# Optimization experiments

Measured on AMD Instinct MI355X. Metric: run time of the kernel, lower is better.

The kernel has to match this reference:

```python
import jax, jax.numpy as jnp
import numpy as np

D_MODEL = 1024
NUM_HEADS = 16
HEAD_DIM = D_MODEL // NUM_HEADS
THETA = 10000.0
B, S = 2, 2048


def setup_inputs() -> dict:
    key = jax.random.key(0)
    ks = jax.random.split(key, 9)
    std = 1.0 / np.sqrt(D_MODEL)
    x = jax.random.normal(ks[0], (B, S, D_MODEL), dtype=jnp.float32)
    Wq = jax.random.normal(ks[1], (D_MODEL, D_MODEL), dtype=jnp.float32) * std
    Wk = jax.random.normal(ks[2], (D_MODEL, D_MODEL), dtype=jnp.float32) * std
    Wv = jax.random.normal(ks[3], (D_MODEL, D_MODEL), dtype=jnp.float32) * std
    Wo = jax.random.normal(ks[4], (D_MODEL, D_MODEL), dtype=jnp.float32) * std
    bq = jax.random.normal(ks[5], (D_MODEL,), dtype=jnp.float32) * std
    bk = jax.random.normal(ks[6], (D_MODEL,), dtype=jnp.float32) * std
    bv = jax.random.normal(ks[7], (D_MODEL,), dtype=jnp.float32) * std
    bo = jax.random.normal(ks[8], (D_MODEL,), dtype=jnp.float32) * std
    return {"x": x, "Wq": Wq, "bq": bq, "Wk": Wk, "bk": bk,
            "Wv": Wv, "bv": bv, "Wo": Wo, "bo": bo}


def _apply_rope(t, cos, sin):
    # t: [B, H, S, hd]; cos/sin: [S, hd//2]; interleaved-pair rotation
    t1 = t[..., 0::2]
    t2 = t[..., 1::2]
    r1 = t1 * cos - t2 * sin
    r2 = t1 * sin + t2 * cos
    return jnp.stack([r1, r2], axis=-1).reshape(t.shape)


def reference(x, Wq, bq, Wk, bk, Wv, bv, Wo, bo):
    B_, S_, D = x.shape
    H, hd = NUM_HEADS, HEAD_DIM
    # QKV projections (nn.Linear: x @ W.T + b)
    q = (x @ Wq.T + bq).reshape(B_, S_, H, hd).transpose(0, 2, 1, 3)  # [B,H,S,hd]
    k = (x @ Wk.T + bk).reshape(B_, S_, H, hd).transpose(0, 2, 1, 3)
    v = (x @ Wv.T + bv).reshape(B_, S_, H, hd).transpose(0, 2, 1, 3)
    # RoPE with token_positions = arange(S)
    pos = jnp.arange(S_, dtype=jnp.float32)
    inv_freq = 1.0 / (THETA ** (jnp.arange(0, hd, 2, dtype=jnp.float32) / hd))
    ang = pos[:, None] * inv_freq[None, :]  # [S, hd//2]
    cos, sin = jnp.cos(ang), jnp.sin(ang)
    q = _apply_rope(q, cos, sin)
    k = _apply_rope(k, cos, sin)
    # causal scaled-dot-product attention
    scores = jnp.einsum('bhqd,bhkd->bhqk', q, k) / jnp.sqrt(jnp.asarray(hd, x.dtype))
    causal = jnp.arange(S_)[:, None] >= jnp.arange(S_)[None, :]  # [S,S]
    scores = jnp.where(causal, scores, -jnp.inf)
    attn = jax.nn.softmax(scores, axis=-1)
    out = jnp.einsum('bhqk,bhkd->bhqd', attn, v)  # [B,H,S,hd]
    out = out.transpose(0, 2, 1, 3).reshape(B_, S_, D)
    return out @ Wo.T + bo
```

## Files before the change

kernel.cpp:

```cpp
#include <hip/hip_runtime.h>
#include <hip/hip_bf16.h>
#include <stdint.h>

typedef __bf16 bf16_t;
typedef __bf16 bf16x4 __attribute__((ext_vector_type(4)));
typedef __bf16 bf16x8 __attribute__((ext_vector_type(8)));
typedef float  f32x4  __attribute__((ext_vector_type(4)));

#define DM    1024
#define NH    16
#define HD    64
#define SEQ   2048
#define BATCH 2
#define BS    (BATCH*SEQ)
#define NQKV  (3*DM)

#define GLOAD_LDS16(g, l) \
  __builtin_amdgcn_global_load_lds((const __attribute__((address_space(1))) void*)(g), \
                                   (__attribute__((address_space(3))) void*)(l), 16, 0, 0)

__device__ __forceinline__ f32x4 mfma16(bf16x8 a, bf16x8 b, f32x4 c) {
  return __builtin_amdgcn_mfma_f32_16x16x32_bf16(a, b, c, 0, 0, 0);
}

__device__ __forceinline__ bf16x8 vcat(uint2 a, uint2 b) {
  union { uint32_t w[4]; bf16x8 v; } u;
  u.w[0] = a.x; u.w[1] = a.y; u.w[2] = b.x; u.w[3] = b.y;
  return u.v;
}

__global__ __launch_bounds__(256) void k_cast_all(
    const float* __restrict__ x,  const float* __restrict__ Wq,
    const float* __restrict__ Wk, const float* __restrict__ Wv,
    const float* __restrict__ Wo, const float* __restrict__ bq,
    const float* __restrict__ bk, const float* __restrict__ bv,
    bf16_t* __restrict__ xb, bf16_t* __restrict__ Wcat,
    bf16_t* __restrict__ Wob, float* __restrict__ bcat,
    float2* __restrict__ rt)
{
  const int bid = blockIdx.x, tid = threadIdx.x;
  if (bid >= 4099) {
    const int idx = (bid - 4099) * 256 + tid;
    const int s = idx >> 5, i = idx & 31;
    float inv = powf(10000.0f, -(float)(2 * i) / 64.0f);
    float ang = (float)s * inv;
    rt[idx] = make_float2(cosf(ang), sinf(ang));
    return;
  }
  if (bid >= 4096) {
    const int k = bid - 4096;
    const float* src = (k == 0) ? bq : (k == 1) ? bk : bv;
    *(float4*)&bcat[k * DM + tid * 4] = *(const float4*)&src[tid * 4];
    return;
  }
  const float* src; bf16_t* dst; int i;
  if (bid < 2048)      { src = x;  dst = xb;                i = bid * 2048 + tid * 8; }
  else if (bid < 2560) { src = Wq; dst = Wcat;              i = (bid - 2048) * 2048 + tid * 8; }
  else if (bid < 3072) { src = Wk; dst = Wcat + DM * DM;    i = (bid - 2560) * 2048 + tid * 8; }
  else if (bid < 3584) { src = Wv; dst = Wcat + 2 * DM * DM;i = (bid - 3072) * 2048 + tid * 8; }
  else                 { src = Wo; dst = Wob;               i = (bid - 3584) * 2048 + tid * 8; }
  float4 a = *(const float4*)(src + i);
  float4 b = *(const float4*)(src + i + 4);
  bf16x8 o;
  o[0] = (bf16_t)a.x; o[1] = (bf16_t)a.y; o[2] = (bf16_t)a.z; o[3] = (bf16_t)a.w;
  o[4] = (bf16_t)b.x; o[5] = (bf16_t)b.y; o[6] = (bf16_t)b.z; o[7] = (bf16_t)b.w;
  *(bf16x8*)(dst + i) = o;
}

__global__ __launch_bounds__(256) void k_gemm_qk(
    const bf16_t* __restrict__ A, const bf16_t* __restrict__ B,
    const float* __restrict__ bias, const float2* __restrict__ rt,
    bf16_t* __restrict__ Qo, bf16_t* __restrict__ Ko)
{
  const int K = DM;
  __shared__ __align__(16) bf16_t As[128 * 32];
  __shared__ __align__(16) bf16_t Bs[128 * 32];
  const int tid  = threadIdx.x;
  const int lane = tid & 63;
  const int wave = tid >> 6;
  const int wr = wave >> 1, wc = wave & 1;
  const int m0 = blockIdx.y * 128, n0 = blockIdx.x * 128;
  const int c16 = lane & 15, g = lane >> 4;

  f32x4 acc[4][4];
  #pragma unroll
  for (int i = 0; i < 4; ++i)
    #pragma unroll
    for (int j = 0; j < 4; ++j)
      #pragma unroll
      for (int e = 0; e < 4; ++e) acc[i][j][e] = 0.0f;

  const int srow = wave * 32;
  const int lrow = lane >> 2;
  const int lk   = (lane & 3) * 8;
  const bf16_t* ga0 = A + (size_t)(m0 + srow +      lrow) * K + lk;
  const bf16_t* ga1 = A + (size_t)(m0 + srow + 16 + lrow) * K + lk;
  const bf16_t* gb0 = B + (size_t)(n0 + srow +      lrow) * K + lk;
  const bf16_t* gb1 = B + (size_t)(n0 + srow + 16 + lrow) * K + lk;
  bf16_t* la0 = &As[(srow)      * 32];
  bf16_t* la1 = &As[(srow + 16) * 32];
  bf16_t* lb0 = &Bs[(srow)      * 32];
  bf16_t* lb1 = &Bs[(srow + 16) * 32];

  const bf16_t* pa = &As[(wr * 64 + c16) * 32 + g * 8];
  const bf16_t* pb = &Bs[(wc * 64 + c16) * 32 + g * 8];

  for (int kt = 0; kt < K; kt += 32) {
    GLOAD_LDS16(ga0 + kt, la0);
    GLOAD_LDS16(ga1 + kt, la1);
    GLOAD_LDS16(gb0 + kt, lb0);
    GLOAD_LDS16(gb1 + kt, lb1);
    __syncthreads();
    bf16x8 af[4], bfr[4];
    #pragma unroll
    for (int t = 0; t < 4; ++t) af[t]  = *(const bf16x8*)(pa + t * 16 * 32);
    #pragma unroll
    for (int t = 0; t < 4; ++t) bfr[t] = *(const bf16x8*)(pb + t * 16 * 32);
    #pragma unroll
    for (int i = 0; i < 4; ++i)
      #pragma unroll
      for (int j = 0; j < 4; ++j)
        acc[i][j] = mfma16(bfr[j], af[i], acc[i][j]);
    __syncthreads();
  }

  const int region = n0 >> 10;
  bf16_t* dst = region ? Ko : Qo;
  const float qs = region ? 1.0f : (0.125f * 1.44269504088896f);
  #pragma unroll
  for (int j = 0; j < 4; ++j) {
    const int nb = n0 + wc * 64 + j * 16 + (g << 2);
    const float4 bv = *(const float4*)&bias[nb];
    const int h  = (nb >> 6) & 15;
    const int d0 = nb & 63;
    #pragma unroll
    for (int i = 0; i < 4; ++i) {
      const int m = m0 + wr * 64 + i * 16 + c16;
      const int s = m & 2047;
      const int bh = ((m >> 11) << 4) + h;
      const float4 cs = *(const float4*)&rt[(size_t)s * 32 + (d0 >> 1)];
      const float v0 = acc[i][j][0] + bv.x;
      const float v1 = acc[i][j][1] + bv.y;
      const float v2 = acc[i][j][2] + bv.z;
      const float v3 = acc[i][j][3] + bv.w;
      bf16x4 ov;
      ov[0] = (bf16_t)((v0 * cs.x - v1 * cs.y) * qs);
      ov[1] = (bf16_t)((v0 * cs.y + v1 * cs.x) * qs);
      ov[2] = (bf16_t)((v2 * cs.z - v3 * cs.w) * qs);
      ov[3] = (bf16_t)((v2 * cs.w + v3 * cs.z) * qs);
      *(bf16x4*)&dst[((size_t)bh * SEQ + s) * HD + d0] = ov;
    }
  }
}

__global__ __launch_bounds__(256) void k_gemm_v(
    const bf16_t* __restrict__ A, const bf16_t* __restrict__ B,
    const float* __restrict__ bias, bf16_t* __restrict__ Vt)
{
  const int K = DM;
  __shared__ __align__(16) bf16_t As[128 * 32];
  __shared__ __align__(16) bf16_t Bs[128 * 32];
  const int tid  = threadIdx.x;
  const int lane = tid & 63;
  const int wave = tid >> 6;
  const int wr = wave >> 1, wc = wave & 1;
  const int m0 = blockIdx.y * 128, n0 = blockIdx.x * 128;
  const int c16 = lane & 15, g = lane >> 4;

  f32x4 acc[4][4];
  #pragma unroll
  for (int i = 0; i < 4; ++i)
    #pragma unroll
    for (int j = 0; j < 4; ++j)
      #pragma unroll
      for (int e = 0; e < 4; ++e) acc[i][j][e] = 0.0f;

  const int srow = wave * 32;
  const int lrow = lane >> 2;
  const int lk   = (lane & 3) * 8;
  const bf16_t* ga0 = A + (size_t)(m0 + srow +      lrow) * K + lk;
  const bf16_t* ga1 = A + (size_t)(m0 + srow + 16 + lrow) * K + lk;
  const bf16_t* gb0 = B + (size_t)(n0 + srow +      lrow) * K + lk;
  const bf16_t* gb1 = B + (size_t)(n0 + srow + 16 + lrow) * K + lk;
  bf16_t* la0 = &As[(srow)      * 32];
  bf16_t* la1 = &As[(srow + 16) * 32];
  bf16_t* lb0 = &Bs[(srow)      * 32];
  bf16_t* lb1 = &Bs[(srow + 16) * 32];

  const bf16_t* pa = &As[(wr * 64 + c16) * 32 + g * 8];
  const bf16_t* pb = &Bs[(wc * 64 + c16) * 32 + g * 8];

  for (int kt = 0; kt < K; kt += 32) {
    GLOAD_LDS16(ga0 + kt, la0);
    GLOAD_LDS16(ga1 + kt, la1);
    GLOAD_LDS16(gb0 + kt, lb0);
    GLOAD_LDS16(gb1 + kt, lb1);
    __syncthreads();
    bf16x8 af[4], bfr[4];
    #pragma unroll
    for (int t = 0; t < 4; ++t) af[t]  = *(const bf16x8*)(pa + t * 16 * 32);
    #pragma unroll
    for (int t = 0; t < 4; ++t) bfr[t] = *(const bf16x8*)(pb + t * 16 * 32);
    #pragma unroll
    for (int i = 0; i < 4; ++i)
      #pragma unroll
      for (int j = 0; j < 4; ++j)
        acc[i][j] = mfma16(af[i], bfr[j], acc[i][j]);
    __syncthreads();
  }

  const int rbase = m0 + wr * 64 + (g << 2);
  const int cbase = n0 + wc * 64 + c16;
  #pragma unroll
  for (int j = 0; j < 4; ++j) {
    const int c = cbase + j * 16;
    const float bv = bias[c];
    const int h = (c >> 6) & 15;
    const int d = c & 63;
    #pragma unroll
    for (int i = 0; i < 4; ++i) {
      bf16x4 ov;
      #pragma unroll
      for (int e = 0; e < 4; ++e) ov[e] = (bf16_t)(acc[i][j][e] + bv);
      const int r0 = rbase + i * 16;
      const int bh = ((r0 >> 11) << 4) + h;
      *(bf16x4*)&Vt[((size_t)bh * HD + d) * SEQ + (r0 & 2047)] = ov;
    }
  }
}

__global__ __launch_bounds__(512) void k_gemm_out(
    const bf16_t* __restrict__ A, const bf16_t* __restrict__ B,
    const float* __restrict__ bias, float* __restrict__ C)
{
  const int K = DM, N = DM;
  __shared__ __align__(16) bf16_t As[128 * 32];
  __shared__ __align__(16) bf16_t Bs[128 * 32];
  const int tid  = threadIdx.x;
  const int lane = tid & 63;
  const int w    = tid >> 6;
  const int wr = w >> 2, wc = w & 3;
  const int m0 = blockIdx.y * 128, n0 = blockIdx.x * 128;
  const int c16 = lane & 15, g = lane >> 4;

  f32x4 acc[4][2];
  #pragma unroll
  for (int i = 0; i < 4; ++i)
    #pragma unroll
    for (int j = 0; j < 2; ++j)
      #pragma unroll
      for (int e = 0; e < 4; ++e) acc[i][j][e] = 0.0f;

  const int lrow = lane >> 2;
  const int lk   = (lane & 3) * 8;
  const bf16_t* ga = A + (size_t)(m0 + w * 16 + lrow) * K + lk;
  const bf16_t* gb = B + (size_t)(n0 + w * 16 + lrow) * K + lk;
  bf16_t* la = &As[(w * 16) * 32];
  bf16_t* lb = &Bs[(w * 16) * 32];

  const bf16_t* pa = &As[(wr * 64 + c16) * 32 + g * 8];
  const bf16_t* pb = &Bs[(wc * 32 + c16) * 32 + g * 8];

  for (int kt = 0; kt < K; kt += 32) {
    GLOAD_LDS16(ga + kt, la);
    GLOAD_LDS16(gb + kt, lb);
    __syncthreads();
    bf16x8 af[4], bfr[2];
    #pragma unroll
    for (int t = 0; t < 4; ++t) af[t]  = *(const bf16x8*)(pa + t * 16 * 32);
    #pragma unroll
    for (int t = 0; t < 2; ++t) bfr[t] = *(const bf16x8*)(pb + t * 16 * 32);
    #pragma unroll
    for (int i = 0; i < 4; ++i)
      #pragma unroll
      for (int j = 0; j < 2; ++j)
        acc[i][j] = mfma16(af[i], bfr[j], acc[i][j]);
    __syncthreads();
  }

  const int rbase = m0 + wr * 64 + (g << 2);
  const int cbase = n0 + wc * 32 + c16;
  #pragma unroll
  for (int j = 0; j < 2; ++j) {
    const int c = cbase + j * 16;
    const float bv = bias[c];
    #pragma unroll
    for (int i = 0; i < 4; ++i) {
      #pragma unroll
      for (int e = 0; e < 4; ++e) {
        const int r = rbase + i * 16 + e;
        C[(size_t)r * N + c] = acc[i][j][e] + bv;
      }
    }
  }
}

__global__ __launch_bounds__(256, 4) void k_attn(
    const bf16_t* __restrict__ Q, const bf16_t* __restrict__ K,
    const bf16_t* __restrict__ Vt, bf16_t* __restrict__ O)
{
  __shared__ __align__(16) bf16_t kbuf[2][64 * 64];
  __shared__ __align__(16) bf16_t vbuf[2][64 * 64];
  const int tid = threadIdx.x, lane = tid & 63, w = tid >> 6;
  const int qt = 31 - (blockIdx.x >> 5);
  const int bh = blockIdx.x & 31;
  const int b  = bh >> 4, h = bh & 15;
  const int q0 = qt * 64 + w * 16;
  const int c16 = lane & 15;
  const int g   = lane >> 4;
  const int q   = q0 + c16;

  const bf16_t* Qb = Q  + (size_t)bh * SEQ * HD;
  const bf16_t* Kb = K  + (size_t)bh * SEQ * HD;
  const bf16_t* Vb = Vt + (size_t)bh * HD * SEQ;

  bf16x8 qf0 = *(const bf16x8*)&Qb[(size_t)q * HD + g * 8];
  bf16x8 qf1 = *(const bf16x8*)&Qb[(size_t)q * HD + 32 + g * 8];

  f32x4 oacc[4];
  #pragma unroll
  for (int dblk = 0; dblk < 4; ++dblk)
    #pragma unroll
    for (int e = 0; e < 4; ++e) oacc[dblk][e] = 0.0f;
  float m_ = -1e30f, l_ = 0.0f;

  const int ntile = qt + 1;

  const int soff0 = w * 1024 + lane * 16;
  const int soff1 = soff0 + 4096;
  const int srow0 = soff0 >> 7, srow1 = soff1 >> 7;
  const int scb0  = (soff0 & 127) ^ ((srow0 & 7) << 4);
  const int scb1  = (soff1 & 127) ^ ((srow1 & 7) << 4);
  const bf16_t* gk0 = &Kb[(size_t)srow0 * HD + (scb0 >> 1)];
  const bf16_t* gk1 = &Kb[(size_t)srow1 * HD + (scb1 >> 1)];
  const bf16_t* gv0 = &Vb[(size_t)srow0 * SEQ + (scb0 >> 1)];
  const bf16_t* gv1 = &Vb[(size_t)srow1 * SEQ + (scb1 >> 1)];
  bf16_t* lk0A = &kbuf[0][(w * 1024) >> 1];
  bf16_t* lk1A = &kbuf[0][(w * 1024 + 4096) >> 1];
  bf16_t* lk0B = &kbuf[1][(w * 1024) >> 1];
  bf16_t* lk1B = &kbuf[1][(w * 1024 + 4096) >> 1];
  bf16_t* lv0A = &vbuf[0][(w * 1024) >> 1];
  bf16_t* lv1A = &vbuf[0][(w * 1024 + 4096) >> 1];
  bf16_t* lv0B = &vbuf[1][(w * 1024) >> 1];
  bf16_t* lv1B = &vbuf[1][(w * 1024 + 4096) >> 1];

  const int sw = (c16 & 7) << 4;
  const int e0 = ((16 * g) ^ sw) >> 1;
  const int dhi = (((64 + 16 * g) ^ sw) >> 1) - e0;
  const bf16_t* kp0 = &kbuf[0][c16 * 64 + e0];
  const bf16_t* kp1 = &kbuf[1][c16 * 64 + e0];
  const int ve0 = ((8 * g) ^ sw) >> 1;
  const int ve1 = ((32 + 8 * g) ^ sw) >> 1;
  const int ve2 = ((64 + 8 * g) ^ sw) >> 1;
  const int ve3 = ((96 + 8 * g) ^ sw) >> 1;
  const bf16_t* vp0 = &vbuf[0][c16 * 64];
  const bf16_t* vp1 = &vbuf[1][c16 * 64];

  GLOAD_LDS16(gk0, lk0A); GLOAD_LDS16(gk1, lk1A);
  GLOAD_LDS16(gv0, lv0A); GLOAD_LDS16(gv1, lv1A);
  gk0 += 4096; gk1 += 4096; gv0 += 64; gv1 += 64;
  __syncthreads();

  for (int t = 0; t < ntile; ++t) {
    const bool odd = t & 1;
    if (t + 1 < ntile) {
      GLOAD_LDS16(gk0, odd ? lk0A : lk0B); GLOAD_LDS16(gk1, odd ? lk1A : lk1B);
      GLOAD_LDS16(gv0, odd ? lv0A : lv0B); GLOAD_LDS16(gv1, odd ? lv1A : lv1B);
      gk0 += 4096; gk1 += 4096; gv0 += 64; gv1 += 64;
    }

    const bf16_t* kp = odd ? kp1 : kp0;
    const bf16_t* vp = odd ? vp1 : vp0;

    f32x4 st[4];
    __builtin_amdgcn_s_setprio(1);
    #pragma unroll
    for (int u = 0; u < 4; ++u) {
      bf16x8 k0 = *(const bf16x8*)(kp + u * 1024);
      bf16x8 k1 = *(const bf16x8*)(kp + u * 1024 + dhi);
      f32x4 z; z[0] = z[1] = z[2] = z[3] = 0.0f;
      z = mfma16(k0, qf0, z);
      z = mfma16(k1, qf1, z);
      st[u] = z;
    }
    __builtin_amdgcn_s_setprio(0);

    bf16x8 vlo[4], vhi[4];
    #pragma unroll
    for (int dblk = 0; dblk < 4; ++dblk) {
      const bf16_t* vpb = vp + dblk * 1024;
      uint2 a0 = *(const uint2*)(vpb + ve0);
      uint2 a1 = *(const uint2*)(vpb + ve1);
      uint2 a2 = *(const uint2*)(vpb + ve2);
      uint2 a3 = *(const uint2*)(vpb + ve3);
      vlo[dblk] = vcat(a0, a1);
      vhi[dblk] = vcat(a2, a3);
    }

    float pv[16];
    if (t == qt) {
      const int kv0 = t * 64;
      #pragma unroll
      for (int u = 0; u < 4; ++u)
        #pragma unroll
        for (int r = 0; r < 4; ++r) {
          const int kv = kv0 + 16 * u + 4 * g + r;
          pv[u * 4 + r] = (kv <= q) ? st[u][r] : -1e30f;
        }
    } else {
      #pragma unroll
      for (int u = 0; u < 4; ++u)
        #pragma unroll
        for (int r = 0; r < 4; ++r)
          pv[u * 4 + r] = st[u][r];
    }

    float ma = fmaxf(fmaxf(pv[0], pv[1]), fmaxf(pv[2], pv[3]));
    float mb = fmaxf(fmaxf(pv[4], pv[5]), fmaxf(pv[6], pv[7]));
    float mc = fmaxf(fmaxf(pv[8], pv[9]), fmaxf(pv[10], pv[11]));
    float md = fmaxf(fmaxf(pv[12], pv[13]), fmaxf(pv[14], pv[15]));
    const float lmx = fmaxf(fmaxf(ma, mb), fmaxf(mc, md));

    if (__any(lmx - m_ > 12.0f)) {
      float mx = fmaxf(lmx, __shfl_xor(lmx, 16));
      mx = fmaxf(mx, __shfl_xor(mx, 32));
      const float mn = fmaxf(m_, mx);
      const float alpha = exp2f(m_ - mn);
      l_ *= alpha;
      #pragma unroll
      for (int dblk = 0; dblk < 4; ++dblk)
        #pragma unroll
        for (int e = 0; e < 4; ++e) oacc[dblk][e] *= alpha;
      m_ = mn;
    }

    #pragma unroll
    for (int i = 0; i < 16; ++i) pv[i] = exp2f(pv[i] - m_);
    float s0 = (pv[0] + pv[1]) + (pv[2] + pv[3]);
    float s1 = (pv[4] + pv[5]) + (pv[6] + pv[7]);
    float s2 = (pv[8] + pv[9]) + (pv[10] + pv[11]);
    float s3 = (pv[12] + pv[13]) + (pv[14] + pv[15]);
    l_ += (s0 + s1) + (s2 + s3);

    bf16x8 pf0, pf1;
    #pragma unroll
    for (int j = 0; j < 8; ++j) {
      pf0[j] = (bf16_t)pv[j];
      pf1[j] = (bf16_t)pv[8 + j];
    }

    __builtin_amdgcn_s_setprio(1);
    #pragma unroll
    for (int dblk = 0; dblk < 4; ++dblk) {
      oacc[dblk] = mfma16(vlo[dblk], pf0, oacc[dblk]);
      oacc[dblk] = mfma16(vhi[dblk], pf1, oacc[dblk]);
    }
    __builtin_amdgcn_s_setprio(0);

    __syncthreads();
  }

  l_ += __shfl_xor(l_, 16);
  l_ += __shfl_xor(l_, 32);
  const float inv = 1.0f / l_;
  bf16_t* orow = O + ((size_t)(b * SEQ + q)) * DM + h * HD;
  #pragma unroll
  for (int dblk = 0; dblk < 4; ++dblk) {
    bf16x4 ov;
    #pragma unroll
    for (int r = 0; r < 4; ++r) ov[r] = (bf16_t)(oacc[dblk][r] * inv);
    *(bf16x4*)&orow[dblk * 16 + 4 * g] = ov;
  }
}

extern "C" void kernel_launch(void* const* d_in, const int* in_sizes, int n_in,
                              void* d_out, int out_size, void* d_ws, size_t ws_size,
                              hipStream_t stream)
{
  const float* x  = (const float*)d_in[0];
  const float* Wq = (const float*)d_in[1];
  const float* bq = (const float*)d_in[2];
  const float* Wk = (const float*)d_in[3];
  const float* bk = (const float*)d_in[4];
  const float* Wv = (const float*)d_in[5];
  const float* bv = (const float*)d_in[6];
  const float* Wo = (const float*)d_in[7];
  const float* bo = (const float*)d_in[8];
  float* out = (float*)d_out;

  char* ws = (char*)d_ws;
  size_t off = 0;
  auto alloc = [&](size_t bytes) { char* p = ws + off; off += (bytes + 255) & ~255ULL; return p; };
  bf16_t* xb   = (bf16_t*)alloc((size_t)BS * DM * 2);
  bf16_t* Wcat = (bf16_t*)alloc((size_t)NQKV * DM * 2);
  bf16_t* Wob  = (bf16_t*)alloc((size_t)DM * DM * 2);
  float*  bcat = (float*)alloc((size_t)NQKV * 4);
  float2* rt   = (float2*)alloc((size_t)SEQ * 32 * 8);
  bf16_t* Qh   = (bf16_t*)alloc((size_t)BS * DM * 2);
  bf16_t* Kh   = (bf16_t*)alloc((size_t)BS * DM * 2);
  bf16_t* Vth  = (bf16_t*)alloc((size_t)BS * DM * 2);
  bf16_t* Oh   = (bf16_t*)alloc((size_t)BS * DM * 2);
  (void)ws_size; (void)in_sizes; (void)n_in; (void)out_size;

  k_cast_all<<<4099 + 256, 256, 0, stream>>>(x, Wq, Wk, Wv, Wo, bq, bk, bv,
                                             xb, Wcat, Wob, bcat, rt);

  dim3 gqk(16, 32);
  k_gemm_qk<<<gqk, 256, 0, stream>>>(xb, Wcat, bcat, rt, Qh, Kh);
  dim3 gv(8, 32);
  k_gemm_v<<<gv, 256, 0, stream>>>(xb, Wcat + 2 * DM * DM, bcat + 2 * DM, Vth);
  k_attn<<<32 * 32, 256, 0, stream>>>(Qh, Kh, Vth, Oh);
  dim3 g2(DM / 128, BS / 128);
  k_gemm_out<<<g2, 512, 0, stream>>>(Oh, Wob, bo, out);
}
```

Measured before the change: 129.5 us.

## Permute V-transpose sequence layout for 16-byte LDS reads; reorder attention tile schedule

The V projection epilogue now writes Vt with a permuted sequence order inside each 64-wide block, so that in the attention kernel each lane's eight needed V elements are contiguous. Each lane can then fetch them with one 16-byte LDS read in place of four 8-byte reads plus a register concatenation. The same swizzle offsets used for K are reused for V. Separately, the mapping from block index to query tile changes from strictly descending to a zig-zag over four rounds, which changes how causal work is spread across the launch order.

```diff
diff --git a/kernel.cpp b/kernel.cpp
--- a/kernel.cpp
+++ b/kernel.cpp
@@ -21,12 +21,6 @@
 
 __device__ __forceinline__ f32x4 mfma16(bf16x8 a, bf16x8 b, f32x4 c) {
   return __builtin_amdgcn_mfma_f32_16x16x32_bf16(a, b, c, 0, 0, 0);
-}
-
-__device__ __forceinline__ bf16x8 vcat(uint2 a, uint2 b) {
-  union { uint32_t w[4]; bf16x8 v; } u;
-  u.w[0] = a.x; u.w[1] = a.y; u.w[2] = b.x; u.w[3] = b.y;
-  return u.v;
 }
 
 __global__ __launch_bounds__(256) void k_cast_all(
@@ -224,7 +218,10 @@
       for (int e = 0; e < 4; ++e) ov[e] = (bf16_t)(acc[i][j][e] + bv);
       const int r0 = rbase + i * 16;
       const int bh = ((r0 >> 11) << 4) + h;
-      *(bf16x4*)&Vt[((size_t)bh * HD + d) * SEQ + (r0 & 2047)] = ov;
+      const int s0 = r0 & 2047;
+      const int u  = (s0 >> 4) & 3;
+      const int p0 = (s0 & ~63) + ((u >> 1) << 5) + (g << 3) + ((u & 1) << 2);
+      *(bf16x4*)&Vt[((size_t)bh * HD + d) * SEQ + p0] = ov;
     }
   }
 }
@@ -302,8 +299,10 @@
   __shared__ __align__(16) bf16_t kbuf[2][64 * 64];
   __shared__ __align__(16) bf16_t vbuf[2][64 * 64];
   const int tid = threadIdx.x, lane = tid & 63, w = tid >> 6;
-  const int qt = 31 - (blockIdx.x >> 5);
+  const int rr = blockIdx.x >> 8;
+  const int kk = (blockIdx.x >> 5) & 7;
   const int bh = blockIdx.x & 31;
+  const int qt = (rr == 0) ? kk : (rr == 1) ? 15 - kk : (rr == 2) ? 16 + kk : 31 - kk;
   const int b  = bh >> 4, h = bh & 15;
   const int q0 = qt * 64 + w * 16;
   const int c16 = lane & 15;
@@ -349,12 +348,8 @@
   const int dhi = (((64 + 16 * g) ^ sw) >> 1) - e0;
   const bf16_t* kp0 = &kbuf[0][c16 * 64 + e0];
   const bf16_t* kp1 = &kbuf[1][c16 * 64 + e0];
-  const int ve0 = ((8 * g) ^ sw) >> 1;
-  const int ve1 = ((32 + 8 * g) ^ sw) >> 1;
-  const int ve2 = ((64 + 8 * g) ^ sw) >> 1;
-  const int ve3 = ((96 + 8 * g) ^ sw) >> 1;
-  const bf16_t* vp0 = &vbuf[0][c16 * 64];
-  const bf16_t* vp1 = &vbuf[1][c16 * 64];
+  const bf16_t* vp0 = &vbuf[0][c16 * 64 + e0];
+  const bf16_t* vp1 = &vbuf[1][c16 * 64 + e0];
 
   GLOAD_LDS16(gk0, lk0A); GLOAD_LDS16(gk1, lk1A);
   GLOAD_LDS16(gv0, lv0A); GLOAD_LDS16(gv1, lv1A);
@@ -388,13 +383,8 @@
     bf16x8 vlo[4], vhi[4];
     #pragma unroll
     for (int dblk = 0; dblk < 4; ++dblk) {
-      const bf16_t* vpb = vp + dblk * 1024;
-      uint2 a0 = *(const uint2*)(vpb + ve0);
-      uint2 a1 = *(const uint2*)(vpb + ve1);
-      uint2 a2 = *(const uint2*)(vpb + ve2);
-      uint2 a3 = *(const uint2*)(vpb + ve3);
-      vlo[dblk] = vcat(a0, a1);
-      vhi[dblk] = vcat(a2, a3);
+      vlo[dblk] = *(const bf16x8*)(vp + dblk * 1024);
+      vhi[dblk] = *(const bf16x8*)(vp + dblk * 1024 + dhi);
     }
 
     float pv[16];
```

After: 126.8 us. -2.1%, faster.
